# Kernel optimization log

Measured on AMD Instinct MI355X. Metric: run time of the kernel, lower is better.

The kernel has to match this reference:

```python
import jax, jax.numpy as jnp
import numpy as np


def _cas(N, dtype=jnp.float32):
    # cas(2*pi*k*n/N) = cos + sin, symmetric NxN matrix (rebuilt per call, as in the original)
    n = jnp.arange(N, dtype=dtype)
    ang = (2.0 * jnp.pi / N) * jnp.outer(n, n)
    return jnp.cos(ang) + jnp.sin(ang)


def dht(x):
    # Discrete Hartley transform over the last axis via dense matmul
    return x @ _cas(x.shape[-1], x.dtype)


def reverse(x):
    # X[(N - k) mod N]: index 0 stays, rest are flipped
    return jnp.roll(jnp.flip(x, axis=-1), 1, axis=-1)


def setup_inputs() -> dict:
    key = jax.random.key(0)
    k1, k2 = jax.random.split(key)
    B, Cin, Cout, N, M = 4, 16, 16, 8192, 64
    x = jax.random.normal(k1, (B, Cin, N), dtype=jnp.float32)
    scale = 1.0 / (Cin * Cout)
    weights1 = scale * jax.random.uniform(k2, (Cin, Cout, M), dtype=jnp.float32)
    return {"x": x, "weights1": weights1}


def reference(x, weights1):
    B, Cin, N = x.shape
    Cout, M = weights1.shape[1], weights1.shape[2]
    N2 = N // 2 + 1

    # DHT of the input over the spatial axis
    x_ht = dht(x)                                   # [B, Cin, N]

    # compl_mul1d on the first `modes1` Hartley coefficients
    hp = dht(x_ht[:, :, :M])                        # [B, Cin, M] (DHT applied again, as in source)
    hq = dht(weights1)                              # [Cin, Cout, M]
    rp = reverse(hp)
    rq = reverse(hq)
    # (t1 + t2 + t3 - t4)/2 == ((hp+rp)@hq + (hp-rp)@rq)/2
    hz = 0.5 * (jnp.einsum('bix,iox->box', hp + rp, hq)
                + jnp.einsum('bix,iox->box', hp - rp, rq))  # [B, Cout, M]
    # idht normalizes by the TOTAL element count of its argument (quirk preserved)
    z = dht(hz) / (B * Cout * M)                    # [B, Cout, M]

    # Scatter into half-spectrum buffer, then idht (imag part is always zero -> stay real)
    out_ht = jnp.zeros((B, Cout, N2), dtype=x.dtype).at[:, :, :M].set(z)
    out = dht(out_ht) / (B * Cout * N2)             # [B, Cout, N//2 + 1]
    return out
```

## Files before the change

### kernel.cpp

```cpp
#include <hip/hip_runtime.h>
#include <math.h>

#define TWO_PI 6.283185307179586f

__global__ __launch_bounds__(256) void kA(const float* __restrict__ x,
                                          float* __restrict__ P) {
  __shared__ float sH[128], cH[128], sL[64], cL[64];
  const int blk = blockIdx.x;
  const int t = threadIdx.x;

  if (t < 128) {
    float s, c;
    __sincosf((float)t * (TWO_PI / 128.0f), &s, &c);
    sH[t] = s;
    cH[t] = c;
  } else if (t < 192) {
    const int g = t - 128;
    float s, c;
    __sincosf((float)g * (TWO_PI / 8192.0f), &s, &c);
    sL[g] = s;
    cL[g] = c;
  }
  __syncthreads();

  const int r  = blk & 63;
  const int mb = (blk >> 6) & 1;
  const int nh = (blk >> 7) & 1;
  const int l  = t & 63;
  const int w  = t >> 6;
  const int mbase = mb * 32 + w * 8;
  const float* xr = x + r * 8192 + nh * 4096;

  float u[8], v[8], Cs[8], Ss[8];
  float accA[8][4];
  float accB[8][3];

#pragma unroll
  for (int q = 0; q < 8; ++q) {
    const int m = mbase + q;
    const int idx0 = ((nh * 4096 + 4 * l) * m) & 8191;
    const int h = idx0 >> 6, g = idx0 & 63;
    const float c0 = cH[h] * cL[g] - sH[h] * sL[g];
    const float s0 = sH[h] * cL[g] + cH[h] * sL[g];
    u[q] = c0 + s0;
    v[q] = c0 - s0;
    const int ih = (4 * m) & 127;
    Cs[q] = cH[ih];
    Ss[q] = sH[ih];
#pragma unroll
    for (int j = 0; j < 4; ++j) accA[q][j] = 0.0f;
#pragma unroll
    for (int j = 0; j < 3; ++j) accB[q][j] = 0.0f;
  }

#pragma unroll 8
  for (int it = 0; it < 16; ++it) {
    const float4 xv = *reinterpret_cast<const float4*>(xr + it * 256 + 4 * l);
#pragma unroll
    for (int q = 0; q < 8; ++q) {
      accA[q][0] += xv.x * u[q];
      accA[q][1] += xv.y * u[q];
      accA[q][2] += xv.z * u[q];
      accA[q][3] += xv.w * u[q];
      accB[q][0] += xv.y * v[q];
      accB[q][1] += xv.z * v[q];
      accB[q][2] += xv.w * v[q];
      const float un = Cs[q] * u[q] + Ss[q] * v[q];
      const float vn = Cs[q] * v[q] - Ss[q] * u[q];
      u[q] = un;
      v[q] = vn;
    }
  }

  float cval, sval;
  {
    const int qq = (l >> 2) & 7;
    const int jj = l & 3;
    const int jm = jj * (mbase + qq);
    const int h = jm >> 6, g = jm & 63;
    cval = cH[h] * cL[g] - sH[h] * sL[g];
    sval = sH[h] * cL[g] + cH[h] * sL[g];
  }

#pragma unroll
  for (int q = 0; q < 8; ++q) {
    float acc = accA[q][0];
#pragma unroll
    for (int j = 1; j < 4; ++j) {
      const float cj = __shfl(cval, q * 4 + j, 64);
      const float sj = __shfl(sval, q * 4 + j, 64);
      acc += cj * accA[q][j] + sj * accB[q][j - 1];
    }
#pragma unroll
    for (int off = 32; off > 0; off >>= 1) acc += __shfl_xor(acc, off, 64);
    if (l == q) P[(r * 64 + (mbase + q)) * 2 + nh] = acc;
  }
}

__global__ __launch_bounds__(256) void kB(const float* __restrict__ P,
                                          const float* __restrict__ w1,
                                          float* __restrict__ z) {
  const int blk = blockIdx.x;
  const int b  = blk >> 6;
  const int o  = (blk >> 2) & 15;
  const int mq = blk & 3;
  __shared__ float sA[16][64];
  __shared__ float sW[16][64];
  __shared__ float red[4][16];
  const int t = threadIdx.x;

  for (int idx = t; idx < 1024; idx += 256) {
    const int i = idx >> 6;
    const int c = idx & 63;
    const float2 pv =
        *reinterpret_cast<const float2*>(&P[(((b * 16 + i) << 6) + c) * 2]);
    sA[i][c] = pv.x + pv.y;
    sW[i][c] = w1[((i * 16 + o) << 6) + c];
  }
  __syncthreads();

  const int w  = t >> 6;
  const int l  = t & 63;
  const int jq = l >> 4;
  const int ml = l & 15;
  const int m  = mq * 16 + ml;

  float acc = 0.0f;
#pragma unroll
  for (int ii = 0; ii < 4; ++ii) {
    const int i = w * 4 + ii;
#pragma unroll
    for (int jb = 0; jb < 4; ++jb) {
      const float4 a4 =
          *reinterpret_cast<const float4*>(&sA[i][jq * 16 + jb * 4]);
      const int j0 = jq * 16 + jb * 4;
      acc += a4.x * sW[i][(m - j0) & 63];
      acc += a4.y * sW[i][(m - j0 - 1) & 63];
      acc += a4.z * sW[i][(m - j0 - 2) & 63];
      acc += a4.w * sW[i][(m - j0 - 3) & 63];
    }
  }
  acc += __shfl_xor(acc, 16, 64);
  acc += __shfl_xor(acc, 32, 64);
  if (jq == 0) red[w][ml] = acc;
  __syncthreads();
  if (t < 16)
    z[(((b * 16 + o) << 6)) + m] =
        (red[0][t] + red[1][t] + red[2][t] + red[3][t]) * (1.0f / 64.0f);
}

__global__ __launch_bounds__(256) void kC(const float* __restrict__ z,
                                          float* __restrict__ out) {
  const int row = blockIdx.x;
  const int kc  = blockIdx.y;
  __shared__ float zr[64];
  const int t = threadIdx.x;
  if (t < 64) zr[t] = z[row * 64 + t];
  __syncthreads();
  const int k = kc * 256 + t;
  if (k >= 4097) return;
  const float th = (float)k * (TWO_PI / 4097.0f);
  float s1, c1;
  __sincosf(th, &s1, &c1);

  float cw[8], sw[8];
  cw[0] = 1.0f; sw[0] = 0.0f;
  cw[1] = c1;   sw[1] = s1;
#pragma unroll
  for (int b = 2; b < 8; ++b) {
    cw[b] = cw[b - 1] * c1 - sw[b - 1] * s1;
    sw[b] = sw[b - 1] * c1 + cw[b - 1] * s1;
  }
  const float c8 = cw[7] * c1 - sw[7] * s1;
  const float s8 = sw[7] * c1 + cw[7] * s1;

  float A[8], B[8];
#pragma unroll
  for (int b = 0; b < 8; ++b) { A[b] = 0.0f; B[b] = 0.0f; }
  float u = 1.0f, v = 1.0f;
#pragma unroll
  for (int a = 0; a < 8; ++a) {
#pragma unroll
    for (int b = 0; b < 8; ++b) {
      const float zz = zr[a * 8 + b];
      A[b] += zz * u;
      B[b] += zz * v;
    }
    const float un = c8 * u + s8 * v;
    const float vn = c8 * v - s8 * u;
    u = un;
    v = vn;
  }
  float acc = 0.0f;
#pragma unroll
  for (int b = 0; b < 8; ++b) acc += cw[b] * A[b] + sw[b] * B[b];
  out[row * 4097 + k] = acc * (1.0f / 262208.0f);
}

extern "C" void kernel_launch(void* const* d_in, const int* in_sizes, int n_in,
                              void* d_out, int out_size, void* d_ws, size_t ws_size,
                              hipStream_t stream) {
  const float* x  = (const float*)d_in[0];
  const float* w1 = (const float*)d_in[1];
  float* out = (float*)d_out;
  float* ws = (float*)d_ws;
  float* P  = ws;
  float* z  = ws + 8192;

  kA<<<256, 256, 0, stream>>>(x, P);
  kB<<<256, 256, 0, stream>>>(P, w1, z);
  kC<<<dim3(64, 17), 256, 0, stream>>>(z, out);
}
```

Baseline: 70.69 us.

## Fuse three stages into one cooperative kernel with a grid-wide sync

Merges the input DHT projection, the mode mixing, and the output inverse DHT into one cooperative kernel with 256 blocks, using a grid sync between the first and later phases. After the sync, each block recomputes one full output row of z in shared memory, so the intermediate z buffer and two kernel launches go away. The output DHT is then spread over 4 blocks per row, each handling 1024 outputs. The cost is redundant mixing work, since every block recomputes its row's 64 coefficients, plus the overhead of a cooperative grid barrier.

```diff
diff --git a/kernel.cpp b/kernel.cpp
--- a/kernel.cpp
+++ b/kernel.cpp
@@ -1,11 +1,56 @@
 #include <hip/hip_runtime.h>
+#include <hip/hip_cooperative_groups.h>
 #include <math.h>
 
 #define TWO_PI 6.283185307179586f
 
-__global__ __launch_bounds__(256) void kA(const float* __restrict__ x,
-                                          float* __restrict__ P) {
+namespace cg = cooperative_groups;
+
+__device__ __forceinline__ float dht4097_row(const float* zr, int k) {
+  const float th = (float)k * (TWO_PI / 4097.0f);
+  float s1, c1;
+  __sincosf(th, &s1, &c1);
+  float cw[8], sw[8];
+  cw[0] = 1.0f; sw[0] = 0.0f;
+  cw[1] = c1;   sw[1] = s1;
+#pragma unroll
+  for (int b = 2; b < 8; ++b) {
+    cw[b] = cw[b - 1] * c1 - sw[b - 1] * s1;
+    sw[b] = sw[b - 1] * c1 + cw[b - 1] * s1;
+  }
+  const float c8 = cw[7] * c1 - sw[7] * s1;
+  const float s8 = sw[7] * c1 + cw[7] * s1;
+  float A[8], B[8];
+#pragma unroll
+  for (int b = 0; b < 8; ++b) { A[b] = 0.0f; B[b] = 0.0f; }
+  float u = 1.0f, v = 1.0f;
+#pragma unroll
+  for (int a = 0; a < 8; ++a) {
+#pragma unroll
+    for (int b = 0; b < 8; ++b) {
+      const float zz = zr[a * 8 + b];
+      A[b] += zz * u;
+      B[b] += zz * v;
+    }
+    const float un = c8 * u + s8 * v;
+    const float vn = c8 * v - s8 * u;
+    u = un; v = vn;
+  }
+  float acc = 0.0f;
+#pragma unroll
+  for (int b = 0; b < 8; ++b) acc += cw[b] * A[b] + sw[b] * B[b];
+  return acc;
+}
+
+__global__ __launch_bounds__(256) void fused(const float* __restrict__ x,
+                                             const float* __restrict__ w1,
+                                             float* __restrict__ out,
+                                             float* __restrict__ P) {
   __shared__ float sH[128], cH[128], sL[64], cL[64];
+  __shared__ float sA[16][64];
+  __shared__ float sW[16][64];
+  __shared__ float zrow[64];
+
   const int blk = blockIdx.x;
   const int t = threadIdx.x;
 
@@ -23,91 +68,87 @@
   }
   __syncthreads();
 
-  const int r  = blk & 63;
-  const int mb = (blk >> 6) & 1;
-  const int nh = (blk >> 7) & 1;
-  const int l  = t & 63;
-  const int w  = t >> 6;
-  const int mbase = mb * 32 + w * 8;
-  const float* xr = x + r * 8192 + nh * 4096;
-
-  float u[8], v[8], Cs[8], Ss[8];
-  float accA[8][4];
-  float accB[8][3];
-
-#pragma unroll
-  for (int q = 0; q < 8; ++q) {
-    const int m = mbase + q;
-    const int idx0 = ((nh * 4096 + 4 * l) * m) & 8191;
-    const int h = idx0 >> 6, g = idx0 & 63;
-    const float c0 = cH[h] * cL[g] - sH[h] * sL[g];
-    const float s0 = sH[h] * cL[g] + cH[h] * sL[g];
-    u[q] = c0 + s0;
-    v[q] = c0 - s0;
-    const int ih = (4 * m) & 127;
-    Cs[q] = cH[ih];
-    Ss[q] = sH[ih];
-#pragma unroll
-    for (int j = 0; j < 4; ++j) accA[q][j] = 0.0f;
-#pragma unroll
-    for (int j = 0; j < 3; ++j) accB[q][j] = 0.0f;
-  }
+  {
+    const int r  = blk & 63;
+    const int mb = (blk >> 6) & 1;
+    const int nh = (blk >> 7) & 1;
+    const int l  = t & 63;
+    const int w  = t >> 6;
+    const int mbase = mb * 32 + w * 8;
+    const float* xr = x + r * 8192 + nh * 4096;
+
+    float u[8], v[8], Cs[8], Ss[8];
+    float accA[8][4];
+    float accB[8][3];
+
+#pragma unroll
+    for (int q = 0; q < 8; ++q) {
+      const int m = mbase + q;
+      const int idx0 = ((nh * 4096 + 4 * l) * m) & 8191;
+      const int h = idx0 >> 6, g = idx0 & 63;
+      const float c0 = cH[h] * cL[g] - sH[h] * sL[g];
+      const float s0 = sH[h] * cL[g] + cH[h] * sL[g];
+      u[q] = c0 + s0;
+      v[q] = c0 - s0;
+      const int ih = (4 * m) & 127;
+      Cs[q] = cH[ih];
+      Ss[q] = sH[ih];
+#pragma unroll
+      for (int j = 0; j < 4; ++j) accA[q][j] = 0.0f;
+#pragma unroll
+      for (int j = 0; j < 3; ++j) accB[q][j] = 0.0f;
+    }
 
 #pragma unroll 8
-  for (int it = 0; it < 16; ++it) {
-    const float4 xv = *reinterpret_cast<const float4*>(xr + it * 256 + 4 * l);
+    for (int it = 0; it < 16; ++it) {
+      const float4 xv = *reinterpret_cast<const float4*>(xr + it * 256 + 4 * l);
+#pragma unroll
+      for (int q = 0; q < 8; ++q) {
+        accA[q][0] += xv.x * u[q];
+        accA[q][1] += xv.y * u[q];
+        accA[q][2] += xv.z * u[q];
+        accA[q][3] += xv.w * u[q];
+        accB[q][0] += xv.y * v[q];
+        accB[q][1] += xv.z * v[q];
+        accB[q][2] += xv.w * v[q];
+        const float un = Cs[q] * u[q] + Ss[q] * v[q];
+        const float vn = Cs[q] * v[q] - Ss[q] * u[q];
+        u[q] = un;
+        v[q] = vn;
+      }
+    }
+
+    float cval, sval;
+    {
+      const int qq = (l >> 2) & 7;
+      const int jj = l & 3;
+      const int jm = jj * (mbase + qq);
+      const int h = jm >> 6, g = jm & 63;
+      cval = cH[h] * cL[g] - sH[h] * sL[g];
+      sval = sH[h] * cL[g] + cH[h] * sL[g];
+    }
+
 #pragma unroll
     for (int q = 0; q < 8; ++q) {
-      accA[q][0] += xv.x * u[q];
-      accA[q][1] += xv.y * u[q];
-      accA[q][2] += xv.z * u[q];
-      accA[q][3] += xv.w * u[q];
-      accB[q][0] += xv.y * v[q];
-      accB[q][1] += xv.z * v[q];
-      accB[q][2] += xv.w * v[q];
-      const float un = Cs[q] * u[q] + Ss[q] * v[q];
-      const float vn = Cs[q] * v[q] - Ss[q] * u[q];
-      u[q] = un;
-      v[q] = vn;
-    }
-  }
-
-  float cval, sval;
-  {
-    const int qq = (l >> 2) & 7;
-    const int jj = l & 3;
-    const int jm = jj * (mbase + qq);
-    const int h = jm >> 6, g = jm & 63;
-    cval = cH[h] * cL[g] - sH[h] * sL[g];
-    sval = sH[h] * cL[g] + cH[h] * sL[g];
-  }
-
-#pragma unroll
-  for (int q = 0; q < 8; ++q) {
-    float acc = accA[q][0];
-#pragma unroll
-    for (int j = 1; j < 4; ++j) {
-      const float cj = __shfl(cval, q * 4 + j, 64);
-      const float sj = __shfl(sval, q * 4 + j, 64);
-      acc += cj * accA[q][j] + sj * accB[q][j - 1];
-    }
-#pragma unroll
-    for (int off = 32; off > 0; off >>= 1) acc += __shfl_xor(acc, off, 64);
-    if (l == q) P[(r * 64 + (mbase + q)) * 2 + nh] = acc;
-  }
-}
-
-__global__ __launch_bounds__(256) void kB(const float* __restrict__ P,
-                                          const float* __restrict__ w1,
-                                          float* __restrict__ z) {
-  const int blk = blockIdx.x;
-  const int b  = blk >> 6;
-  const int o  = (blk >> 2) & 15;
-  const int mq = blk & 3;
-  __shared__ float sA[16][64];
-  __shared__ float sW[16][64];
-  __shared__ float red[4][16];
-  const int t = threadIdx.x;
+      float acc = accA[q][0];
+#pragma unroll
+      for (int j = 1; j < 4; ++j) {
+        const float cj = __shfl(cval, q * 4 + j, 64);
+        const float sj = __shfl(sval, q * 4 + j, 64);
+        acc += cj * accA[q][j] + sj * accB[q][j - 1];
+      }
+#pragma unroll
+      for (int off = 32; off > 0; off >>= 1) acc += __shfl_xor(acc, off, 64);
+      if (l == q) P[(r * 64 + (mbase + q)) * 2 + nh] = acc;
+    }
+  }
+
+  cg::this_grid().sync();
+
+  const int row = blk & 63;
+  const int kq  = blk >> 6;
+  const int b   = row >> 4;
+  const int o   = row & 15;
 
   for (int idx = t; idx < 1024; idx += 256) {
     const int i = idx >> 6;
@@ -119,82 +160,39 @@
   }
   __syncthreads();
 
-  const int w  = t >> 6;
-  const int l  = t & 63;
-  const int jq = l >> 4;
-  const int ml = l & 15;
-  const int m  = mq * 16 + ml;
-
-  float acc = 0.0f;
-#pragma unroll
-  for (int ii = 0; ii < 4; ++ii) {
-    const int i = w * 4 + ii;
-#pragma unroll
-    for (int jb = 0; jb < 4; ++jb) {
-      const float4 a4 =
-          *reinterpret_cast<const float4*>(&sA[i][jq * 16 + jb * 4]);
-      const int j0 = jq * 16 + jb * 4;
-      acc += a4.x * sW[i][(m - j0) & 63];
-      acc += a4.y * sW[i][(m - j0 - 1) & 63];
-      acc += a4.z * sW[i][(m - j0 - 2) & 63];
-      acc += a4.w * sW[i][(m - j0 - 3) & 63];
-    }
-  }
-  acc += __shfl_xor(acc, 16, 64);
-  acc += __shfl_xor(acc, 32, 64);
-  if (jq == 0) red[w][ml] = acc;
+  {
+    const int w  = t >> 6;
+    const int l  = t & 63;
+    const int jq = l >> 4;
+    const int ml = l & 15;
+    const int m  = w * 16 + ml;
+    float acc = 0.0f;
+#pragma unroll
+    for (int i = 0; i < 16; ++i) {
+#pragma unroll
+      for (int jb = 0; jb < 4; ++jb) {
+        const int j0 = jq * 16 + jb * 4;
+        const float4 a4 = *reinterpret_cast<const float4*>(&sA[i][j0]);
+        acc += a4.x * sW[i][(m - j0) & 63];
+        acc += a4.y * sW[i][(m - j0 - 1) & 63];
+        acc += a4.z * sW[i][(m - j0 - 2) & 63];
+        acc += a4.w * sW[i][(m - j0 - 3) & 63];
+      }
+    }
+    acc += __shfl_xor(acc, 16, 64);
+    acc += __shfl_xor(acc, 32, 64);
+    if (jq == 0) zrow[m] = acc * (1.0f / 64.0f);
+  }
   __syncthreads();
-  if (t < 16)
-    z[(((b * 16 + o) << 6)) + m] =
-        (red[0][t] + red[1][t] + red[2][t] + red[3][t]) * (1.0f / 64.0f);
-}
-
-__global__ __launch_bounds__(256) void kC(const float* __restrict__ z,
-                                          float* __restrict__ out) {
-  const int row = blockIdx.x;
-  const int kc  = blockIdx.y;
-  __shared__ float zr[64];
-  const int t = threadIdx.x;
-  if (t < 64) zr[t] = z[row * 64 + t];
-  __syncthreads();
-  const int k = kc * 256 + t;
-  if (k >= 4097) return;
-  const float th = (float)k * (TWO_PI / 4097.0f);
-  float s1, c1;
-  __sincosf(th, &s1, &c1);
-
-  float cw[8], sw[8];
-  cw[0] = 1.0f; sw[0] = 0.0f;
-  cw[1] = c1;   sw[1] = s1;
-#pragma unroll
-  for (int b = 2; b < 8; ++b) {
-    cw[b] = cw[b - 1] * c1 - sw[b - 1] * s1;
-    sw[b] = sw[b - 1] * c1 + cw[b - 1] * s1;
-  }
-  const float c8 = cw[7] * c1 - sw[7] * s1;
-  const float s8 = sw[7] * c1 + cw[7] * s1;
-
-  float A[8], B[8];
-#pragma unroll
-  for (int b = 0; b < 8; ++b) { A[b] = 0.0f; B[b] = 0.0f; }
-  float u = 1.0f, v = 1.0f;
-#pragma unroll
-  for (int a = 0; a < 8; ++a) {
-#pragma unroll
-    for (int b = 0; b < 8; ++b) {
-      const float zz = zr[a * 8 + b];
-      A[b] += zz * u;
-      B[b] += zz * v;
-    }
-    const float un = c8 * u + s8 * v;
-    const float vn = c8 * v - s8 * u;
-    u = un;
-    v = vn;
-  }
-  float acc = 0.0f;
-#pragma unroll
-  for (int b = 0; b < 8; ++b) acc += cw[b] * A[b] + sw[b] * B[b];
-  out[row * 4097 + k] = acc * (1.0f / 262208.0f);
+
+#pragma unroll
+  for (int ch = 0; ch < 4; ++ch) {
+    const int k = kq * 1024 + ch * 256 + t;
+    out[row * 4097 + k] = dht4097_row(zrow, k) * (1.0f / 262208.0f);
+  }
+  if (kq == 3 && t == 0) {
+    out[row * 4097 + 4096] = dht4097_row(zrow, 4096) * (1.0f / 262208.0f);
+  }
 }
 
 extern "C" void kernel_launch(void* const* d_in, const int* in_sizes, int n_in,
@@ -203,11 +201,9 @@
   const float* x  = (const float*)d_in[0];
   const float* w1 = (const float*)d_in[1];
   float* out = (float*)d_out;
-  float* ws = (float*)d_ws;
-  float* P  = ws;
-  float* z  = ws + 8192;
-
-  kA<<<256, 256, 0, stream>>>(x, P);
-  kB<<<256, 256, 0, stream>>>(P, w1, z);
-  kC<<<dim3(64, 17), 256, 0, stream>>>(z, out);
+  float* P   = (float*)d_ws;
+
+  void* args[] = {(void*)&x, (void*)&w1, (void*)&out, (void*)&P};
+  hipLaunchCooperativeKernel((void*)fused, dim3(256), dim3(256), args, 0,
+                             stream);
 }
```

After: 103.6 us. +46.5%, slower.
